# Kernel optimization log

Hardware: AMD Instinct MI355X
Metric: run time of the kernel (lower is better)

## Reference

```python
import jax, jax.numpy as jnp
import numpy as np

B, S, D_IN, D_OUT = 4, 4096, 1024, 64

def setup_inputs() -> dict:
    key = jax.random.key(0)
    ks = jax.random.split(key, 7)
    return {
        "x":  jax.random.normal(ks[0], (B, S, D_IN), dtype=jnp.float32),
        "Wq": jax.random.normal(ks[1], (D_IN, D_OUT), dtype=jnp.float32) * 0.02,
        "bq": jax.random.normal(ks[2], (D_OUT,), dtype=jnp.float32) * 0.02,
        "Wk": jax.random.normal(ks[3], (D_IN, D_OUT), dtype=jnp.float32) * 0.02,
        "bk": jax.random.normal(ks[4], (D_OUT,), dtype=jnp.float32) * 0.02,
        "Wv": jax.random.normal(ks[5], (D_IN, D_OUT), dtype=jnp.float32) * 0.02,
        "bv": jax.random.normal(ks[6], (D_OUT,), dtype=jnp.float32) * 0.02,
    }

def reference(x, Wq, bq, Wk, bk, Wv, bv):
    # x: [B, S, d_in]
    seq = x.shape[1]
    q = x @ Wq + bq            # [B, S, d_out]
    k = x @ Wk + bk
    v = x @ Wv + bv
    scores = jnp.einsum("bqd,bkd->bqk", q, k)          # [B, S, S]
    causal = jnp.triu(jnp.ones((seq, seq), dtype=bool), k=1)
    scores = jnp.where(causal[None, :, :], -jnp.inf, scores)
    # NOTE: original code scales by sqrt(token_len), not sqrt(d_out) (d_k = keys.shape[1])
    scale = jnp.sqrt(jnp.asarray(seq, dtype=scores.dtype))
    attn = jax.nn.softmax(scores / scale, axis=-1)      # [B, S, S]
    # dropout in the original is applied but its result is discarded -> no-op
    return jnp.einsum("bqk,bkd->bqd", attn, v)          # [B, S, d_out]
```

## Files before the change

kernel.cpp:

```cpp
#include <hip/hip_runtime.h>
#include <math.h>

#define B 4
#define S 4096
#define DIN 1024
#define DOUT 64
#define BS (B * S)

typedef __bf16 bf16;
typedef __bf16 bf16x4 __attribute__((ext_vector_type(4)));
typedef __bf16 bf16x8 __attribute__((ext_vector_type(8)));
typedef float f32x4 __attribute__((ext_vector_type(4)));

#define QSCALE 0.022542110013890053f

#define QS_OFF 0
#define K_OFF  (2u * 1024 * 1024)
#define VT_OFF (4u * 1024 * 1024)
#define WP_OFF (6u * 1024 * 1024)
#define OP_OFF (7u * 1024 * 1024)
#define LP_OFF (15u * 1024 * 1024)

__global__ __launch_bounds__(256) void wpack_kernel(
    const float* __restrict__ Wq, const float* __restrict__ Wk,
    const float* __restrict__ Wv, bf16* __restrict__ wp) {
  const int t = blockIdx.x * 256 + threadIdx.x;
  const int m = t >> 16;
  const int r = t & 65535;
  const int k = r >> 6;
  const int n64 = r & 63;
  const float* W = (m == 0) ? Wq : (m == 1) ? Wk : Wv;
  const float v = W[r];
  const int n = m * 64 + n64;
  const int nt = n >> 4;
  const int lane = ((k >> 3) & 3) * 16 + (n & 15);
  const int idx = ((nt * 32 + (k >> 5)) * 64 + lane) * 8 + (k & 7);
  wp[idx] = (bf16)v;
}

__global__ __launch_bounds__(256) void qkv_mfma_kernel(
    const float* __restrict__ x, const float* __restrict__ bq,
    const float* __restrict__ bk, const float* __restrict__ bv,
    const bf16* __restrict__ wp, bf16* __restrict__ Qs,
    bf16* __restrict__ Kb, bf16* __restrict__ VT) {
  __shared__ float part[3][12][64][4];

  const int wid = threadIdx.x >> 6;
  const int lane = threadIdx.x & 63;
  const int l15 = lane & 15;
  const int quad = lane >> 4;
  const int strip = blockIdx.x;

  const float* xrow =
      x + (size_t)(strip * 16 + l15) * DIN + quad * 8 + wid * 256;
  const bf16x8* wp8 = (const bf16x8*)wp;

  f32x4 acc[12];
#pragma unroll
  for (int nt = 0; nt < 12; ++nt) acc[nt] = (f32x4)(0.f);

#pragma unroll
  for (int kc = 0; kc < 8; ++kc) {
    const float4 a0 = *(const float4*)(xrow + kc * 32);
    const float4 a1 = *(const float4*)(xrow + kc * 32 + 4);
    bf16x8 af;
    af[0] = (bf16)a0.x; af[1] = (bf16)a0.y; af[2] = (bf16)a0.z; af[3] = (bf16)a0.w;
    af[4] = (bf16)a1.x; af[5] = (bf16)a1.y; af[6] = (bf16)a1.z; af[7] = (bf16)a1.w;
#pragma unroll
    for (int nt = 0; nt < 12; ++nt) {
      const bf16x8 bfr = wp8[(nt * 32 + wid * 8 + kc) * 64 + lane];
      acc[nt] = __builtin_amdgcn_mfma_f32_16x16x32_bf16(af, bfr, acc[nt], 0, 0, 0);
    }
  }

  if (wid != 0) {
#pragma unroll
    for (int nt = 0; nt < 12; ++nt)
      *(f32x4*)&part[wid - 1][nt][lane][0] = acc[nt];
  }
  __syncthreads();
  if (wid == 0) {
#pragma unroll
    for (int nt = 0; nt < 12; ++nt) {
#pragma unroll
      for (int w = 0; w < 3; ++w) {
        const f32x4 p = *(const f32x4*)&part[w][nt][lane][0];
        acc[nt] += p;
      }
    }
#pragma unroll
    for (int nt = 0; nt < 12; ++nt) {
      const int sel = nt >> 2;
      const int c = (nt & 3) * 16 + l15;
      const float* bb = (sel == 0) ? bq : (sel == 1) ? bk : bv;
      const float bias = bb[c];
      if (sel == 2) {
        const int b = strip >> 8;
        const int s0 = (strip & 255) * 16 + quad * 4;
        bf16x4 vv;
#pragma unroll
        for (int r = 0; r < 4; ++r) vv[r] = (bf16)(acc[nt][r] + bias);
        *(bf16x4*)(VT + ((size_t)b * DOUT + c) * S + s0) = vv;
      } else {
        const float scale = (sel == 0) ? QSCALE : 1.f;
        bf16* ob = (sel == 0) ? Qs : Kb;
#pragma unroll
        for (int r = 0; r < 4; ++r) {
          const int row = strip * 16 + quad * 4 + r;
          ob[(size_t)row * DOUT + c] = (bf16)((acc[nt][r] + bias) * scale);
        }
      }
    }
  }
}

__global__ __launch_bounds__(256, 4) void attn_mfma_kernel(
    const bf16* __restrict__ Qs, const bf16* __restrict__ Kb,
    const bf16* __restrict__ VT, bf16* __restrict__ Oh,
    float* __restrict__ lh) {
  __shared__ __align__(16) bf16 kt[64][72];
  __shared__ __align__(16) bf16 vt[64][72];
  __shared__ __align__(16) bf16 pw[4][16][72];

  const int tid = threadIdx.x;
  const int wid = tid >> 6;
  const int lane = tid & 63;
  const int l15 = lane & 15;
  const int quad = lane >> 4;
  const int b = blockIdx.x & 3;
  const int quarter = (blockIdx.x >> 2) & 3;
  const int strip = 63 - (blockIdx.x >> 4);
  const int ntiles = strip + 1;
  const int t0 = (quarter * ntiles) >> 2;
  const int t1 = ((quarter + 1) * ntiles) >> 2;

  const bf16* Qb = Qs + ((size_t)b * S + strip * 64 + wid * 16) * DOUT;
  const bf16* Kbase = Kb + (size_t)b * S * DOUT;
  const bf16* VTb = VT + (size_t)b * DOUT * S;

  const bf16x8 qf0 = *(const bf16x8*)(Qb + l15 * DOUT + quad * 8);
  const bf16x8 qf1 = *(const bf16x8*)(Qb + l15 * DOUT + 32 + quad * 8);

  const int c0 = tid * 2, c1 = tid * 2 + 1;
  const int r0 = c0 >> 3, q0 = (c0 & 7) * 8;
  const int r1 = c1 >> 3, q1 = (c1 & 7) * 8;

  f32x4 o[4];
#pragma unroll
  for (int i = 0; i < 4; ++i) o[i] = (f32x4)(0.f);
  f32x4 lsum = (f32x4)(0.f);

  bf16x8 kg0, kg1, vg0, vg1;
  if (t0 < t1) {
    const bf16* Kt = Kbase + (size_t)t0 * 64 * DOUT;
    kg0 = *(const bf16x8*)(Kt + r0 * DOUT + q0);
    kg1 = *(const bf16x8*)(Kt + r1 * DOUT + q1);
    vg0 = *(const bf16x8*)(VTb + (size_t)r0 * S + t0 * 64 + q0);
    vg1 = *(const bf16x8*)(VTb + (size_t)r1 * S + t0 * 64 + q1);
  }

  for (int t = t0; t < t1; ++t) {
    __syncthreads();
    *(bf16x8*)&kt[r0][q0] = kg0;
    *(bf16x8*)&kt[r1][q1] = kg1;
    *(bf16x8*)&vt[r0][q0] = vg0;
    *(bf16x8*)&vt[r1][q1] = vg1;
    if (t + 1 < t1) {
      const bf16* Kt = Kbase + (size_t)(t + 1) * 64 * DOUT;
      kg0 = *(const bf16x8*)(Kt + r0 * DOUT + q0);
      kg1 = *(const bf16x8*)(Kt + r1 * DOUT + q1);
      vg0 = *(const bf16x8*)(VTb + (size_t)r0 * S + (t + 1) * 64 + q0);
      vg1 = *(const bf16x8*)(VTb + (size_t)r1 * S + (t + 1) * 64 + q1);
    }
    __syncthreads();

    bf16x8 kf[8];
#pragma unroll
    for (int nt = 0; nt < 4; ++nt)
#pragma unroll
      for (int c = 0; c < 2; ++c)
        kf[nt * 2 + c] = *(const bf16x8*)&kt[nt * 16 + l15][c * 32 + quad * 8];

    f32x4 s[4];
#pragma unroll
    for (int nt = 0; nt < 4; ++nt) {
      s[nt] = __builtin_amdgcn_mfma_f32_16x16x32_bf16(qf0, kf[nt * 2 + 0],
                                                      (f32x4)(0.f), 0, 0, 0);
      s[nt] = __builtin_amdgcn_mfma_f32_16x16x32_bf16(qf1, kf[nt * 2 + 1],
                                                      s[nt], 0, 0, 0);
    }

    if (t == ntiles - 1) {
#pragma unroll
      for (int nt = 0; nt < 4; ++nt) {
        const int key = t * 64 + nt * 16 + l15;
#pragma unroll
        for (int r = 0; r < 4; ++r) {
          const int qrow = strip * 64 + wid * 16 + quad * 4 + r;
          const float p = (key <= qrow) ? exp2f(fminf(s[nt][r], 44.f)) : 0.f;
          lsum[r] += p;
          pw[wid][quad * 4 + r][nt * 16 + l15] = (bf16)p;
        }
      }
    } else {
#pragma unroll
      for (int nt = 0; nt < 4; ++nt)
#pragma unroll
        for (int r = 0; r < 4; ++r) {
          const float p = exp2f(fminf(s[nt][r], 44.f));
          lsum[r] += p;
          pw[wid][quad * 4 + r][nt * 16 + l15] = (bf16)p;
        }
    }

    const bf16x8 pf0 = *(const bf16x8*)&pw[wid][l15][quad * 8];
    const bf16x8 pf1 = *(const bf16x8*)&pw[wid][l15][32 + quad * 8];

#pragma unroll
    for (int ntd = 0; ntd < 4; ++ntd) {
      const bf16x8 vf0 = *(const bf16x8*)&vt[ntd * 16 + l15][quad * 8];
      const bf16x8 vf1 = *(const bf16x8*)&vt[ntd * 16 + l15][32 + quad * 8];
      o[ntd] = __builtin_amdgcn_mfma_f32_16x16x32_bf16(pf0, vf0, o[ntd], 0, 0, 0);
      o[ntd] = __builtin_amdgcn_mfma_f32_16x16x32_bf16(pf1, vf1, o[ntd], 0, 0, 0);
    }
  }

#pragma unroll
  for (int m = 1; m < 16; m <<= 1)
#pragma unroll
    for (int r = 0; r < 4; ++r) lsum[r] += __shfl_xor(lsum[r], m, 64);

  const int slot = (b * 64 + strip) * 4 + quarter;
  if (l15 == 0) {
#pragma unroll
    for (int r = 0; r < 4; ++r)
      lh[slot * 64 + wid * 16 + quad * 4 + r] = lsum[r];
  }
#pragma unroll
  for (int ntd = 0; ntd < 4; ++ntd)
#pragma unroll
    for (int r = 0; r < 4; ++r)
      Oh[(size_t)slot * 4096 + (wid * 16 + quad * 4 + r) * 64 + ntd * 16 + l15] =
          (bf16)o[ntd][r];
}

__global__ __launch_bounds__(256) void combine_kernel(
    const bf16* __restrict__ Oh, const float* __restrict__ lh,
    float* __restrict__ out) {
  const int gid = blockIdx.x * 256 + threadIdx.x;
  const int token = gid >> 4;
  const int d4 = (gid & 15) * 4;
  const int bq = token >> 12;
  const int s = token & 4095;
  const int strip = s >> 6;
  const int qq = s & 63;
  const int slot0 = (bq * 64 + strip) * 4;
  f32x4 acc = (f32x4)(0.f);
  float l = 0.f;
#pragma unroll
  for (int q = 0; q < 4; ++q) {
    const bf16x4 ov =
        *(const bf16x4*)(Oh + (size_t)(slot0 + q) * 4096 + qq * 64 + d4);
#pragma unroll
    for (int i = 0; i < 4; ++i) acc[i] += (float)ov[i];
    l += lh[(slot0 + q) * 64 + qq];
  }
  ((f32x4*)out)[gid] = acc * (1.f / l);
}

extern "C" void kernel_launch(void* const* d_in, const int* in_sizes, int n_in,
                              void* d_out, int out_size, void* d_ws,
                              size_t ws_size, hipStream_t stream) {
  const float* x  = (const float*)d_in[0];
  const float* Wq = (const float*)d_in[1];
  const float* bq = (const float*)d_in[2];
  const float* Wk = (const float*)d_in[3];
  const float* bk = (const float*)d_in[4];
  const float* Wv = (const float*)d_in[5];
  const float* bv = (const float*)d_in[6];
  float* out = (float*)d_out;

  char* ws = (char*)d_ws;
  bf16* Qs = (bf16*)(ws + QS_OFF);
  bf16* Kb = (bf16*)(ws + K_OFF);
  bf16* VT = (bf16*)(ws + VT_OFF);
  bf16* wp = (bf16*)(ws + WP_OFF);
  bf16* Oh = (bf16*)(ws + OP_OFF);
  float* lh = (float*)(ws + LP_OFF);

  wpack_kernel<<<768, 256, 0, stream>>>(Wq, Wk, Wv, wp);
  qkv_mfma_kernel<<<1024, 256, 0, stream>>>(x, bq, bk, bv, wp, Qs, Kb, VT);
  attn_mfma_kernel<<<1024, 256, 0, stream>>>(Qs, Kb, VT, Oh, lh);
  combine_kernel<<<1024, 256, 0, stream>>>(Oh, lh, out);
}
```

Baseline: 157.5 us.

## Restructure QKV projection: split N across waves with double-buffered shared x tiles

The QKV projection kernel now processes 32 rows per block instead of 16. Each wave owns 3 of the 12 output column tiles across the full K dimension, instead of splitting K across waves and reducing partial sums through shared memory. The x tile is staged cooperatively into double-buffered shared memory as bf16, with the next chunk prefetched into registers, so each weight fragment is reused across two row sub-tiles. This removes the cross-wave reduction and halves weight reads per row, but adds 32 barrier-synchronised iterations and halves the grid to 512 blocks.

Result: faster. 148.2 us (-5.9%).

```diff
diff --git a/kernel.cpp b/kernel.cpp
--- a/kernel.cpp
+++ b/kernel.cpp
@@ -43,72 +43,84 @@
     const float* __restrict__ bk, const float* __restrict__ bv,
     const bf16* __restrict__ wp, bf16* __restrict__ Qs,
     bf16* __restrict__ Kb, bf16* __restrict__ VT) {
-  __shared__ float part[3][12][64][4];
-
-  const int wid = threadIdx.x >> 6;
-  const int lane = threadIdx.x & 63;
+  __shared__ __align__(16) bf16 xt[2][32][40];
+
+  const int tid = threadIdx.x;
+  const int wid = tid >> 6;
+  const int lane = tid & 63;
   const int l15 = lane & 15;
   const int quad = lane >> 4;
-  const int strip = blockIdx.x;
-
-  const float* xrow =
-      x + (size_t)(strip * 16 + l15) * DIN + quad * 8 + wid * 256;
+  const int blk = blockIdx.x;
+
+  const int srow = tid >> 3;
+  const int scol = (tid & 7) * 4;
+  const float* xs = x + (size_t)(blk * 32 + srow) * DIN + scol;
   const bf16x8* wp8 = (const bf16x8*)wp;
 
-  f32x4 acc[12];
-#pragma unroll
-  for (int nt = 0; nt < 12; ++nt) acc[nt] = (f32x4)(0.f);
-
-#pragma unroll
-  for (int kc = 0; kc < 8; ++kc) {
-    const float4 a0 = *(const float4*)(xrow + kc * 32);
-    const float4 a1 = *(const float4*)(xrow + kc * 32 + 4);
-    bf16x8 af;
-    af[0] = (bf16)a0.x; af[1] = (bf16)a0.y; af[2] = (bf16)a0.z; af[3] = (bf16)a0.w;
-    af[4] = (bf16)a1.x; af[5] = (bf16)a1.y; af[6] = (bf16)a1.z; af[7] = (bf16)a1.w;
-#pragma unroll
-    for (int nt = 0; nt < 12; ++nt) {
-      const bf16x8 bfr = wp8[(nt * 32 + wid * 8 + kc) * 64 + lane];
-      acc[nt] = __builtin_amdgcn_mfma_f32_16x16x32_bf16(af, bfr, acc[nt], 0, 0, 0);
-    }
-  }
-
-  if (wid != 0) {
-#pragma unroll
-    for (int nt = 0; nt < 12; ++nt)
-      *(f32x4*)&part[wid - 1][nt][lane][0] = acc[nt];
-  }
+  f32x4 acc[3][2];
+#pragma unroll
+  for (int j = 0; j < 3; ++j)
+#pragma unroll
+    for (int st = 0; st < 2; ++st) acc[j][st] = (f32x4)(0.f);
+
+  {
+    const float4 r0 = *(const float4*)(xs);
+    bf16x4 c;
+    c[0] = (bf16)r0.x; c[1] = (bf16)r0.y; c[2] = (bf16)r0.z; c[3] = (bf16)r0.w;
+    *(bf16x4*)&xt[0][srow][scol] = c;
+  }
+  float4 rn = *(const float4*)(xs + 32);
   __syncthreads();
-  if (wid == 0) {
-#pragma unroll
-    for (int nt = 0; nt < 12; ++nt) {
-#pragma unroll
-      for (int w = 0; w < 3; ++w) {
-        const f32x4 p = *(const f32x4*)&part[w][nt][lane][0];
-        acc[nt] += p;
-      }
-    }
-#pragma unroll
-    for (int nt = 0; nt < 12; ++nt) {
-      const int sel = nt >> 2;
-      const int c = (nt & 3) * 16 + l15;
-      const float* bb = (sel == 0) ? bq : (sel == 1) ? bk : bv;
-      const float bias = bb[c];
+
+  for (int kc = 0; kc < 32; ++kc) {
+    const int buf = kc & 1;
+
+    bf16x8 bfr[3];
+#pragma unroll
+    for (int j = 0; j < 3; ++j)
+      bfr[j] = wp8[((wid * 3 + j) * 32 + kc) * 64 + lane];
+
+    const bf16x8 a0 = *(const bf16x8*)&xt[buf][l15][quad * 8];
+    const bf16x8 a1 = *(const bf16x8*)&xt[buf][16 + l15][quad * 8];
+
+#pragma unroll
+    for (int j = 0; j < 3; ++j) {
+      acc[j][0] = __builtin_amdgcn_mfma_f32_16x16x32_bf16(a0, bfr[j], acc[j][0], 0, 0, 0);
+      acc[j][1] = __builtin_amdgcn_mfma_f32_16x16x32_bf16(a1, bfr[j], acc[j][1], 0, 0, 0);
+    }
+
+    if (kc + 1 < 32) {
+      bf16x4 c;
+      c[0] = (bf16)rn.x; c[1] = (bf16)rn.y; c[2] = (bf16)rn.z; c[3] = (bf16)rn.w;
+      *(bf16x4*)&xt[buf ^ 1][srow][scol] = c;
+      if (kc + 2 < 32) rn = *(const float4*)(xs + (kc + 2) * 32);
+    }
+    __syncthreads();
+  }
+
+#pragma unroll
+  for (int j = 0; j < 3; ++j) {
+    const int nt = wid * 3 + j;
+    const int sel = nt >> 2;
+    const int c = (nt & 3) * 16 + l15;
+    const float* bb = (sel == 0) ? bq : (sel == 1) ? bk : bv;
+    const float bias = bb[c];
+#pragma unroll
+    for (int st = 0; st < 2; ++st) {
+      const int row0 = blk * 32 + st * 16 + quad * 4;
       if (sel == 2) {
-        const int b = strip >> 8;
-        const int s0 = (strip & 255) * 16 + quad * 4;
+        const int b = row0 >> 12;
+        const int s0 = row0 & 4095;
         bf16x4 vv;
 #pragma unroll
-        for (int r = 0; r < 4; ++r) vv[r] = (bf16)(acc[nt][r] + bias);
+        for (int r = 0; r < 4; ++r) vv[r] = (bf16)(acc[j][st][r] + bias);
         *(bf16x4*)(VT + ((size_t)b * DOUT + c) * S + s0) = vv;
       } else {
         const float scale = (sel == 0) ? QSCALE : 1.f;
         bf16* ob = (sel == 0) ? Qs : Kb;
 #pragma unroll
-        for (int r = 0; r < 4; ++r) {
-          const int row = strip * 16 + quad * 4 + r;
-          ob[(size_t)row * DOUT + c] = (bf16)((acc[nt][r] + bias) * scale);
-        }
+        for (int r = 0; r < 4; ++r)
+          ob[(size_t)(row0 + r) * DOUT + c] = (bf16)((acc[j][st][r] + bias) * scale);
       }
     }
   }
@@ -289,7 +301,7 @@
   float* lh = (float*)(ws + LP_OFF);
 
   wpack_kernel<<<768, 256, 0, stream>>>(Wq, Wk, Wv, wp);
-  qkv_mfma_kernel<<<1024, 256, 0, stream>>>(x, bq, bk, bv, wp, Qs, Kb, VT);
+  qkv_mfma_kernel<<<512, 256, 0, stream>>>(x, bq, bk, bv, wp, Qs, Kb, VT);
   attn_mfma_kernel<<<1024, 256, 0, stream>>>(Qs, Kb, VT, Oh, lh);
   combine_kernel<<<1024, 256, 0, stream>>>(Oh, lh, out);
 }
```
